# Kernel optimization log

Measured on AMD Instinct MI355X. Metric: run time of the kernel, lower is better.

## Reference

```python
import jax, jax.numpy as jnp
import numpy as np

N_NODES = 50000
N_EDGES = 800000
D_FEAT = 128      # node feature dim (== coef_dim)
COEF_DIM = 128
OUT_DIM = 128     # node_layer / neighbour_layer output dim
EPS = 1e-12       # tf.math.l2_normalize epsilon


def setup_inputs() -> dict:
    key = jax.random.key(0)
    ks = jax.random.split(key, 8)
    s = 1.0 / np.sqrt(D_FEAT)
    h = jax.random.normal(ks[0], (N_NODES, D_FEAT), dtype=jnp.float32)
    src = jax.random.randint(ks[1], (N_EDGES,), 0, N_NODES, dtype=jnp.int32)
    dst = jax.random.randint(ks[2], (N_EDGES,), 0, N_NODES, dtype=jnp.int32)
    W_coef = jax.random.normal(ks[3], (D_FEAT, COEF_DIM), dtype=jnp.float32) * s
    b_coef = jnp.zeros((COEF_DIM,), dtype=jnp.float32)
    W_red = jax.random.normal(ks[4], (2 * COEF_DIM, 1), dtype=jnp.float32) * (1.0 / np.sqrt(2 * COEF_DIM))
    b_red = jnp.zeros((1,), dtype=jnp.float32)
    W_node = jax.random.normal(ks[5], (D_FEAT, OUT_DIM), dtype=jnp.float32) * s
    b_node = jnp.zeros((OUT_DIM,), dtype=jnp.float32)
    W_neigh = jax.random.normal(ks[6], (D_FEAT, OUT_DIM), dtype=jnp.float32) * s
    b_neigh = jnp.zeros((OUT_DIM,), dtype=jnp.float32)
    return {"h": h, "src": src, "dst": dst,
            "W_coef": W_coef, "b_coef": b_coef,
            "W_red": W_red, "b_red": b_red,
            "W_node": W_node, "b_node": b_node,
            "W_neigh": W_neigh, "b_neigh": b_neigh}


def reference(h, src, dst, W_coef, b_coef, W_red, b_red, W_node, b_node, W_neigh, b_neigh):
    n = h.shape[0]
    # message func: per-edge coef transform of source features (activation=None)
    q = h @ W_coef + b_coef                      # [N, C] dst-side coef features
    m = q[src]                                   # [E, C] (coef_layer(h[src]))
    # reduce func: attention score per edge from concat(dst coef, message)
    e = jnp.concatenate([q[dst], m], axis=-1) @ W_red + b_red   # [E, 1]
    e = e[:, 0]
    # softmax over incoming edges of each destination node (stable)
    emax = jax.ops.segment_max(e, dst, num_segments=n)          # [N]
    ex = jnp.exp(e - emax[dst])                                 # [E]
    denom = jax.ops.segment_sum(ex, dst, num_segments=n)        # [N]
    alpha = ex / (denom[dst] + EPS)                             # [E]
    # weighted neighbour aggregation of raw source features ('neigh' mailbox)
    agg = jax.ops.segment_sum(alpha[:, None] * h[src], dst, num_segments=n)  # [N, D]
    # new_h = concat(node_layer(h), neighbour_layer(agg))
    new_h = jnp.concatenate([h @ W_node + b_node, agg @ W_neigh + b_neigh], axis=-1)  # [N, 2*OUT]
    # tf.math.l2_normalize along last axis
    sq = jnp.sum(new_h * new_h, axis=-1, keepdims=True)
    return new_h * jax.lax.rsqrt(jnp.maximum(sq, EPS))
```

## Files before the change

kernel.cpp:

```cpp
#include <hip/hip_runtime.h>
#include <hip/hip_bf16.h>
#include <math.h>

#define N_NODES 50000
#define N_EDGES 800000
#define D_FEAT  128
#define EPSF    1e-12f

#define NPG     120
#define NG      417
#define CHUNK_E 4096
#define NCHUNK  196
#define GCAP    2560

#define OFF_U2      0
#define OFF_GCUR    1024
#define OFF_S       4096
#define OFF_ROWPTR  204800
#define OFF_WTN     405504
#define OFF_WTG     438272
#define OFF_SSRC    471040
#define OFF_HB      3671040
#define OFF_BUCKET  16471040

typedef __attribute__((ext_vector_type(8))) short bf8;
typedef __attribute__((ext_vector_type(4))) float f4;

__global__ void make_u2_kernel(const float* __restrict__ W_coef,
                               const float* __restrict__ W_red,
                               float* __restrict__ u2, int* __restrict__ gcursor) {
    __shared__ float wr[128];
    int k = threadIdx.x;
    wr[k] = W_red[128 + k];
    for (int i = k; i < NG; i += 128) gcursor[i] = 0;
    __syncthreads();
    const float4* row = (const float4*)(W_coef + k * 128);
    float acc = 0.f;
    #pragma unroll
    for (int j = 0; j < 32; ++j) {
        float4 v = row[j];
        acc += v.x * wr[4*j] + v.y * wr[4*j+1] + v.z * wr[4*j+2] + v.w * wr[4*j+3];
    }
    u2[k] = acc;
}

__global__ __launch_bounds__(256) void prep_kernel(
        const float* __restrict__ h, const float* __restrict__ u2,
        const float* __restrict__ Wn, const float* __restrict__ Wg,
        const int* __restrict__ src, const int* __restrict__ dst,
        float* __restrict__ s, unsigned short* __restrict__ hb,
        unsigned short* __restrict__ WtN, unsigned short* __restrict__ WtG,
        int* __restrict__ gcursor, int* __restrict__ bucket) {
    int b = blockIdx.x;
    if (b < 12500) {
        int node = b * 4 + (threadIdx.x >> 6);
        int lane = threadIdx.x & 63;
        float2 hv = ((const float2*)(h + (size_t)node * 128))[lane];
        float2 uv = ((const float2*)u2)[lane];
        float v = hv.x * uv.x + hv.y * uv.y;
        #pragma unroll
        for (int off = 32; off; off >>= 1) v += __shfl_xor(v, off);
        if (lane == 0) s[node] = v;
        __hip_bfloat162 p = __float22bfloat162_rn(hv);
        ((unsigned int*)(hb + (size_t)node * 128))[lane] = *(unsigned int*)&p;
    } else if (b < 12564) {
        int idx = (b - 12500) * 256 + threadIdx.x;
        int n = idx >> 7, k = idx & 127;
        __hip_bfloat16 a = __float2bfloat16(Wn[k * 128 + n]);
        __hip_bfloat16 g = __float2bfloat16(Wg[k * 128 + n]);
        WtN[n * 128 + k] = *(unsigned short*)&a;
        WtG[n * 128 + k] = *(unsigned short*)&g;
    } else {
        __shared__ int lh[NG];
        __shared__ int base[NG];
        __shared__ int cnt2[NG];
        int chunk = b - 12564;
        int tid = threadIdx.x;
        for (int i = tid; i < NG; i += 256) { lh[i] = 0; cnt2[i] = 0; }
        __syncthreads();
        int base_e = chunk * CHUNK_E;
        #pragma unroll
        for (int it = 0; it < CHUNK_E / 256; ++it) {
            int e = base_e + it * 256 + tid;
            if (e < N_EDGES) atomicAdd(&lh[(unsigned)dst[e] / NPG], 1);
        }
        __syncthreads();
        for (int i = tid; i < NG; i += 256) {
            int c = lh[i];
            base[i] = c ? atomicAdd(&gcursor[i], c) : 0;
        }
        __syncthreads();
        #pragma unroll
        for (int it = 0; it < CHUNK_E / 256; ++it) {
            int e = base_e + it * 256 + tid;
            if (e < N_EDGES) {
                int d = dst[e];
                int g = (unsigned)d / NPG;
                int r = atomicAdd(&cnt2[g], 1);
                int p = base[g] + r;
                if (p < GCAP)
                    bucket[(size_t)g * GCAP + p] = src[e] | ((d - g * NPG) << 16);
            }
        }
    }
}

__global__ __launch_bounds__(128) void fine_kernel(
        const int* __restrict__ gcnt, const int* __restrict__ bucket,
        int* __restrict__ row_ptr, int* __restrict__ ssrc) {
    __shared__ int cnt[NPG];
    __shared__ int cnt2[NPG];
    __shared__ int sexcl[NPG];
    __shared__ int ws[2];
    __shared__ int red[2];
    int g = blockIdx.x, tid = threadIdx.x;
    int lane = tid & 63, wid = tid >> 6;

    int partial = 0;
    for (int i = tid; i < g; i += 128) partial += gcnt[i];
    #pragma unroll
    for (int off = 32; off; off >>= 1) partial += __shfl_down(partial, off);
    if (lane == 0) red[wid] = partial;
    if (tid < NPG) { cnt[tid] = 0; cnt2[tid] = 0; }
    __syncthreads();
    int beg = red[0] + red[1];
    int cnt_g = min(gcnt[g], GCAP);
    const int* bk = bucket + (size_t)g * GCAP;

    for (int i = tid; i < cnt_g; i += 128)
        atomicAdd(&cnt[bk[i] >> 16], 1);
    __syncthreads();
    int v = (tid < NPG) ? cnt[tid] : 0;
    int incl = v;
    #pragma unroll
    for (int off = 1; off < 64; off <<= 1) {
        int t = __shfl_up(incl, off);
        if (lane >= off) incl += t;
    }
    if (lane == 63) ws[wid] = incl;
    __syncthreads();
    if (wid == 1) incl += ws[0];
    int excl = incl - v;
    if (tid < NPG) sexcl[tid] = excl;
    int node = g * NPG + tid;
    if (tid < NPG && node < N_NODES) row_ptr[node] = beg + excl;
    if (g == NG - 1 && tid == 0) row_ptr[N_NODES] = N_EDGES;
    __syncthreads();
    for (int i = tid; i < cnt_g; i += 128) {
        int p = bk[i];
        int loc = p >> 16;
        int r = atomicAdd(&cnt2[loc], 1);
        ssrc[beg + sexcl[loc] + r] = p & 0xFFFF;
    }
}

__global__ __launch_bounds__(256) void agg_gemm_kernel(
        const int* __restrict__ row_ptr, const int* __restrict__ ssrc,
        const float* __restrict__ s, const unsigned short* __restrict__ hb,
        const unsigned short* __restrict__ WtN, const unsigned short* __restrict__ WtG,
        const float* __restrict__ b_node, const float* __restrict__ b_neigh,
        float* __restrict__ out) {
    __shared__ __align__(16) unsigned short aggt[16][136];
    __shared__ float ssrp[4][16];
    int wave = threadIdx.x >> 6, lane = threadIdx.x & 63;
    int node0 = blockIdx.x * 16;
    int q = lane >> 4, l16 = lane & 15;

    for (int i = 0; i < 4; ++i) {
        int node = node0 + wave * 4 + i;
        int beg = row_ptr[node];
        int deg = row_ptr[node + 1] - beg;
        float acc[8] = {0.f, 0.f, 0.f, 0.f, 0.f, 0.f, 0.f, 0.f};
        float denom = 0.f;
        for (int base = 0; base < deg; base += 64) {
            int cntv = min(64, deg - base);
            int esrc = 0;
            float w_l = 0.f;
            if (lane < cntv) {
                esrc = ssrc[beg + base + lane];
                w_l = __expf(s[esrc]);
            }
            denom += w_l;
            int groups = (cntv + 3) >> 2;
            for (int j = 0; j < groups; ++j) {
                int e = 4 * j + q;
                int ec = min(e, cntv - 1);
                int bsrc = __shfl(esrc, ec);
                float wv = __shfl(w_l, ec);
                if (e >= cntv) wv = 0.f;
                uint4 hv = *(const uint4*)(hb + (size_t)bsrc * 128 + l16 * 8);
                acc[0] = fmaf(wv, __uint_as_float(hv.x << 16),        acc[0]);
                acc[1] = fmaf(wv, __uint_as_float(hv.x & 0xFFFF0000u), acc[1]);
                acc[2] = fmaf(wv, __uint_as_float(hv.y << 16),        acc[2]);
                acc[3] = fmaf(wv, __uint_as_float(hv.y & 0xFFFF0000u), acc[3]);
                acc[4] = fmaf(wv, __uint_as_float(hv.z << 16),        acc[4]);
                acc[5] = fmaf(wv, __uint_as_float(hv.z & 0xFFFF0000u), acc[5]);
                acc[6] = fmaf(wv, __uint_as_float(hv.w << 16),        acc[6]);
                acc[7] = fmaf(wv, __uint_as_float(hv.w & 0xFFFF0000u), acc[7]);
            }
        }
        #pragma unroll
        for (int t = 0; t < 8; ++t) {
            acc[t] += __shfl_xor(acc[t], 16);
            acc[t] += __shfl_xor(acc[t], 32);
        }
        #pragma unroll
        for (int off = 32; off; off >>= 1) denom += __shfl_xor(denom, off);
        float inv = 1.f / (denom + EPSF);
        if (q == 0) {
            unsigned o[4];
            #pragma unroll
            for (int j2 = 0; j2 < 4; ++j2) {
                __hip_bfloat162 p = __float22bfloat162_rn(
                    make_float2(acc[2*j2] * inv, acc[2*j2+1] * inv));
                o[j2] = *(unsigned*)&p;
            }
            *(uint4*)&aggt[wave * 4 + i][l16 * 8] = make_uint4(o[0], o[1], o[2], o[3]);
        }
    }
    __syncthreads();

    int arow = node0 + l16;
    f4 accN[2], accG[2];
    accN[0] = (f4){0.f,0.f,0.f,0.f}; accN[1] = (f4){0.f,0.f,0.f,0.f};
    accG[0] = (f4){0.f,0.f,0.f,0.f}; accG[1] = (f4){0.f,0.f,0.f,0.f};
    #pragma unroll
    for (int kc = 0; kc < 4; ++kc) {
        int kbase = kc * 32 + q * 8;
        bf8 aH = *(const bf8*)(hb + (size_t)arow * 128 + kbase);
        bf8 aG = *(const bf8*)&aggt[l16][kbase];
        #pragma unroll
        for (int tt = 0; tt < 2; ++tt) {
            int t = wave * 2 + tt;
            bf8 bN = *(const bf8*)(WtN + (size_t)(t * 16 + l16) * 128 + kbase);
            bf8 bG = *(const bf8*)(WtG + (size_t)(t * 16 + l16) * 128 + kbase);
            accN[tt] = __builtin_amdgcn_mfma_f32_16x16x32_bf16(aH, bN, accN[tt], 0, 0, 0);
            accG[tt] = __builtin_amdgcn_mfma_f32_16x16x32_bf16(aG, bG, accG[tt], 0, 0, 0);
        }
    }

    float ssr[4] = {0.f, 0.f, 0.f, 0.f};
    #pragma unroll
    for (int tt = 0; tt < 2; ++tt) {
        int t = wave * 2 + tt;
        float bn = b_node[t * 16 + l16];
        float bg = b_neigh[t * 16 + l16];
        #pragma unroll
        for (int r = 0; r < 4; ++r) {
            accN[tt][r] += bn;
            accG[tt][r] += bg;
            ssr[r] = fmaf(accN[tt][r], accN[tt][r], ssr[r]);
            ssr[r] = fmaf(accG[tt][r], accG[tt][r], ssr[r]);
        }
    }
    #pragma unroll
    for (int r = 0; r < 4; ++r) {
        ssr[r] += __shfl_xor(ssr[r], 1);
        ssr[r] += __shfl_xor(ssr[r], 2);
        ssr[r] += __shfl_xor(ssr[r], 4);
        ssr[r] += __shfl_xor(ssr[r], 8);
    }
    if (l16 == 0) {
        #pragma unroll
        for (int r = 0; r < 4; ++r) ssrp[wave][q * 4 + r] = ssr[r];
    }
    __syncthreads();
    #pragma unroll
    for (int r = 0; r < 4; ++r) {
        float tot = ssrp[0][q*4+r] + ssrp[1][q*4+r] + ssrp[2][q*4+r] + ssrp[3][q*4+r];
        float sc = rsqrtf(fmaxf(tot, EPSF));
        size_t node = node0 + q * 4 + r;
        float* o = out + node * 256;
        #pragma unroll
        for (int tt = 0; tt < 2; ++tt) {
            int t = wave * 2 + tt;
            o[t * 16 + l16]       = accN[tt][r] * sc;
            o[128 + t * 16 + l16] = accG[tt][r] * sc;
        }
    }
}

extern "C" void kernel_launch(void* const* d_in, const int* in_sizes, int n_in,
                              void* d_out, int out_size, void* d_ws, size_t ws_size,
                              hipStream_t stream) {
    const float* h       = (const float*)d_in[0];
    const int*   src     = (const int*)d_in[1];
    const int*   dst     = (const int*)d_in[2];
    const float* W_coef  = (const float*)d_in[3];
    const float* W_red   = (const float*)d_in[5];
    const float* W_node  = (const float*)d_in[7];
    const float* b_node  = (const float*)d_in[8];
    const float* W_neigh = (const float*)d_in[9];
    const float* b_neigh = (const float*)d_in[10];
    float* out = (float*)d_out;

    char* w = (char*)d_ws;
    float*          u2      = (float*)(w + OFF_U2);
    int*            gcursor = (int*)(w + OFF_GCUR);
    float*          s       = (float*)(w + OFF_S);
    int*            row_ptr = (int*)(w + OFF_ROWPTR);
    unsigned short* WtN     = (unsigned short*)(w + OFF_WTN);
    unsigned short* WtG     = (unsigned short*)(w + OFF_WTG);
    int*            ssrc    = (int*)(w + OFF_SSRC);
    unsigned short* hb      = (unsigned short*)(w + OFF_HB);
    int*            bucket  = (int*)(w + OFF_BUCKET);

    make_u2_kernel<<<1, 128, 0, stream>>>(W_coef, W_red, u2, gcursor);
    prep_kernel<<<12500 + 64 + NCHUNK, 256, 0, stream>>>(
        h, u2, W_node, W_neigh, src, dst, s, hb, WtN, WtG, gcursor, bucket);
    fine_kernel<<<NG, 128, 0, stream>>>(gcursor, bucket, row_ptr, ssrc);
    agg_gemm_kernel<<<N_NODES / 16, 256, 0, stream>>>(
        row_ptr, ssrc, s, hb, WtN, WtG, b_node, b_neigh, out);
}
```

Measured before the change: 209.5 us.

## Precompute edge weights in CSR build and use one wave per node

The fine CSR-build kernel now computes exp(s[src]) per edge and stores it next to the source index as an int2, so the aggregation kernel no longer gathers s and evaluates exp. The aggregation kernel grows to 1024 threads per block with one wave per destination node. Each lane handles two feature columns and walks the edges one at a time instead of four per iteration, which removes the cross-quarter shuffle reduction. The GEMM stage gives each of the 16 waves a single 16x16 output tile. The tradeoff is less memory-level parallelism per wave, since there are 4-byte gathers per lane per edge rather than 16-byte ones, plus larger blocks with more waves sitting at the barrier.

```diff
diff --git a/kernel.cpp b/kernel.cpp
--- a/kernel.cpp
+++ b/kernel.cpp
@@ -19,9 +19,9 @@
 #define OFF_ROWPTR  204800
 #define OFF_WTN     405504
 #define OFF_WTG     438272
-#define OFF_SSRC    471040
-#define OFF_HB      3671040
-#define OFF_BUCKET  16471040
+#define OFF_SSRCW   471040
+#define OFF_HB      6871040
+#define OFF_BUCKET  19671040
 
 typedef __attribute__((ext_vector_type(8))) short bf8;
 typedef __attribute__((ext_vector_type(4))) float f4;
@@ -107,7 +107,8 @@
 
 __global__ __launch_bounds__(128) void fine_kernel(
         const int* __restrict__ gcnt, const int* __restrict__ bucket,
-        int* __restrict__ row_ptr, int* __restrict__ ssrc) {
+        const float* __restrict__ s,
+        int* __restrict__ row_ptr, int2* __restrict__ ssrc_w) {
     __shared__ int cnt[NPG];
     __shared__ int cnt2[NPG];
     __shared__ int sexcl[NPG];
@@ -149,109 +150,75 @@
     for (int i = tid; i < cnt_g; i += 128) {
         int p = bk[i];
         int loc = p >> 16;
+        int sv = p & 0xFFFF;
+        float wv = __expf(s[sv]);
         int r = atomicAdd(&cnt2[loc], 1);
-        ssrc[beg + sexcl[loc] + r] = p & 0xFFFF;
-    }
-}
-
-__global__ __launch_bounds__(256) void agg_gemm_kernel(
-        const int* __restrict__ row_ptr, const int* __restrict__ ssrc,
-        const float* __restrict__ s, const unsigned short* __restrict__ hb,
+        ssrc_w[beg + sexcl[loc] + r] = make_int2(sv, __float_as_int(wv));
+    }
+}
+
+__global__ __launch_bounds__(1024) void agg_gemm_kernel(
+        const int* __restrict__ row_ptr, const int2* __restrict__ ssrc_w,
+        const unsigned short* __restrict__ hb,
         const unsigned short* __restrict__ WtN, const unsigned short* __restrict__ WtG,
         const float* __restrict__ b_node, const float* __restrict__ b_neigh,
         float* __restrict__ out) {
     __shared__ __align__(16) unsigned short aggt[16][136];
-    __shared__ float ssrp[4][16];
+    __shared__ float ssrp[16][16];
     int wave = threadIdx.x >> 6, lane = threadIdx.x & 63;
     int node0 = blockIdx.x * 16;
     int q = lane >> 4, l16 = lane & 15;
 
-    for (int i = 0; i < 4; ++i) {
-        int node = node0 + wave * 4 + i;
+    {
+        int node = node0 + wave;
         int beg = row_ptr[node];
         int deg = row_ptr[node + 1] - beg;
-        float acc[8] = {0.f, 0.f, 0.f, 0.f, 0.f, 0.f, 0.f, 0.f};
+        float acc0 = 0.f, acc1 = 0.f;
         float denom = 0.f;
         for (int base = 0; base < deg; base += 64) {
             int cntv = min(64, deg - base);
-            int esrc = 0;
-            float w_l = 0.f;
+            int2 pw = make_int2(0, 0);
+            float wl = 0.f;
             if (lane < cntv) {
-                esrc = ssrc[beg + base + lane];
-                w_l = __expf(s[esrc]);
+                pw = ssrc_w[beg + base + lane];
+                wl = __int_as_float(pw.y);
             }
-            denom += w_l;
-            int groups = (cntv + 3) >> 2;
-            for (int j = 0; j < groups; ++j) {
-                int e = 4 * j + q;
-                int ec = min(e, cntv - 1);
-                int bsrc = __shfl(esrc, ec);
-                float wv = __shfl(w_l, ec);
-                if (e >= cntv) wv = 0.f;
-                uint4 hv = *(const uint4*)(hb + (size_t)bsrc * 128 + l16 * 8);
-                acc[0] = fmaf(wv, __uint_as_float(hv.x << 16),        acc[0]);
-                acc[1] = fmaf(wv, __uint_as_float(hv.x & 0xFFFF0000u), acc[1]);
-                acc[2] = fmaf(wv, __uint_as_float(hv.y << 16),        acc[2]);
-                acc[3] = fmaf(wv, __uint_as_float(hv.y & 0xFFFF0000u), acc[3]);
-                acc[4] = fmaf(wv, __uint_as_float(hv.z << 16),        acc[4]);
-                acc[5] = fmaf(wv, __uint_as_float(hv.z & 0xFFFF0000u), acc[5]);
-                acc[6] = fmaf(wv, __uint_as_float(hv.w << 16),        acc[6]);
-                acc[7] = fmaf(wv, __uint_as_float(hv.w & 0xFFFF0000u), acc[7]);
+            denom += wl;
+            #pragma unroll 4
+            for (int e = 0; e < cntv; ++e) {
+                int bsrc = __shfl(pw.x, e);
+                float wv = __shfl(wl, e);
+                unsigned hv = *(const unsigned*)(hb + (size_t)bsrc * 128 + lane * 2);
+                acc0 = fmaf(wv, __uint_as_float(hv << 16),         acc0);
+                acc1 = fmaf(wv, __uint_as_float(hv & 0xFFFF0000u), acc1);
             }
-        }
-        #pragma unroll
-        for (int t = 0; t < 8; ++t) {
-            acc[t] += __shfl_xor(acc[t], 16);
-            acc[t] += __shfl_xor(acc[t], 32);
         }
         #pragma unroll
         for (int off = 32; off; off >>= 1) denom += __shfl_xor(denom, off);
         float inv = 1.f / (denom + EPSF);
-        if (q == 0) {
-            unsigned o[4];
-            #pragma unroll
-            for (int j2 = 0; j2 < 4; ++j2) {
-                __hip_bfloat162 p = __float22bfloat162_rn(
-                    make_float2(acc[2*j2] * inv, acc[2*j2+1] * inv));
-                o[j2] = *(unsigned*)&p;
-            }
-            *(uint4*)&aggt[wave * 4 + i][l16 * 8] = make_uint4(o[0], o[1], o[2], o[3]);
-        }
-    }
-    __syncthreads();
-
-    int arow = node0 + l16;
-    f4 accN[2], accG[2];
-    accN[0] = (f4){0.f,0.f,0.f,0.f}; accN[1] = (f4){0.f,0.f,0.f,0.f};
-    accG[0] = (f4){0.f,0.f,0.f,0.f}; accG[1] = (f4){0.f,0.f,0.f,0.f};
+        __hip_bfloat162 p = __float22bfloat162_rn(make_float2(acc0 * inv, acc1 * inv));
+        *(unsigned*)&aggt[wave][lane * 2] = *(unsigned*)&p;
+    }
+    __syncthreads();
+
+    int t = wave & 7, half = wave >> 3;
+    const unsigned short* Wt = half ? WtG : WtN;
+    f4 acc = (f4){0.f, 0.f, 0.f, 0.f};
     #pragma unroll
     for (int kc = 0; kc < 4; ++kc) {
         int kbase = kc * 32 + q * 8;
-        bf8 aH = *(const bf8*)(hb + (size_t)arow * 128 + kbase);
-        bf8 aG = *(const bf8*)&aggt[l16][kbase];
-        #pragma unroll
-        for (int tt = 0; tt < 2; ++tt) {
-            int t = wave * 2 + tt;
-            bf8 bN = *(const bf8*)(WtN + (size_t)(t * 16 + l16) * 128 + kbase);
-            bf8 bG = *(const bf8*)(WtG + (size_t)(t * 16 + l16) * 128 + kbase);
-            accN[tt] = __builtin_amdgcn_mfma_f32_16x16x32_bf16(aH, bN, accN[tt], 0, 0, 0);
-            accG[tt] = __builtin_amdgcn_mfma_f32_16x16x32_bf16(aG, bG, accG[tt], 0, 0, 0);
-        }
-    }
-
-    float ssr[4] = {0.f, 0.f, 0.f, 0.f};
-    #pragma unroll
-    for (int tt = 0; tt < 2; ++tt) {
-        int t = wave * 2 + tt;
-        float bn = b_node[t * 16 + l16];
-        float bg = b_neigh[t * 16 + l16];
-        #pragma unroll
-        for (int r = 0; r < 4; ++r) {
-            accN[tt][r] += bn;
-            accG[tt][r] += bg;
-            ssr[r] = fmaf(accN[tt][r], accN[tt][r], ssr[r]);
-            ssr[r] = fmaf(accG[tt][r], accG[tt][r], ssr[r]);
-        }
+        bf8 a = half ? *(const bf8*)&aggt[l16][kbase]
+                     : *(const bf8*)(hb + (size_t)(node0 + l16) * 128 + kbase);
+        bf8 bb = *(const bf8*)(Wt + (size_t)(t * 16 + l16) * 128 + kbase);
+        acc = __builtin_amdgcn_mfma_f32_16x16x32_bf16(a, bb, acc, 0, 0, 0);
+    }
+
+    float bv = (half ? b_neigh : b_node)[t * 16 + l16];
+    float ssr[4];
+    #pragma unroll
+    for (int r = 0; r < 4; ++r) {
+        acc[r] += bv;
+        ssr[r] = acc[r] * acc[r];
     }
     #pragma unroll
     for (int r = 0; r < 4; ++r) {
@@ -267,16 +234,13 @@
     __syncthreads();
     #pragma unroll
     for (int r = 0; r < 4; ++r) {
-        float tot = ssrp[0][q*4+r] + ssrp[1][q*4+r] + ssrp[2][q*4+r] + ssrp[3][q*4+r];
+        int row = q * 4 + r;
+        float tot = 0.f;
+        #pragma unroll
+        for (int w2 = 0; w2 < 16; ++w2) tot += ssrp[w2][row];
         float sc = rsqrtf(fmaxf(tot, EPSF));
-        size_t node = node0 + q * 4 + r;
-        float* o = out + node * 256;
-        #pragma unroll
-        for (int tt = 0; tt < 2; ++tt) {
-            int t = wave * 2 + tt;
-            o[t * 16 + l16]       = accN[tt][r] * sc;
-            o[128 + t * 16 + l16] = accG[tt][r] * sc;
-        }
+        size_t node = node0 + row;
+        out[node * 256 + half * 128 + t * 16 + l16] = acc[r] * sc;
     }
 }
 
@@ -301,14 +265,14 @@
     int*            row_ptr = (int*)(w + OFF_ROWPTR);
     unsigned short* WtN     = (unsigned short*)(w + OFF_WTN);
     unsigned short* WtG     = (unsigned short*)(w + OFF_WTG);
-    int*            ssrc    = (int*)(w + OFF_SSRC);
+    int2*           ssrc_w  = (int2*)(w + OFF_SSRCW);
     unsigned short* hb      = (unsigned short*)(w + OFF_HB);
     int*            bucket  = (int*)(w + OFF_BUCKET);
 
     make_u2_kernel<<<1, 128, 0, stream>>>(W_coef, W_red, u2, gcursor);
     prep_kernel<<<12500 + 64 + NCHUNK, 256, 0, stream>>>(
         h, u2, W_node, W_neigh, src, dst, s, hb, WtN, WtG, gcursor, bucket);
-    fine_kernel<<<NG, 128, 0, stream>>>(gcursor, bucket, row_ptr, ssrc);
-    agg_gemm_kernel<<<N_NODES / 16, 256, 0, stream>>>(
-        row_ptr, ssrc, s, hb, WtN, WtG, b_node, b_neigh, out);
-}
+    fine_kernel<<<NG, 128, 0, stream>>>(gcursor, bucket, s, row_ptr, ssrc_w);
+    agg_gemm_kernel<<<N_NODES / 16, 1024, 0, stream>>>(
+        row_ptr, ssrc_w, hb, WtN, WtG, b_node, b_neigh, out);
+}
```

Result: slower. 249.9 us (+19.3%).
